# Kernel optimization log

Measured on AMD Instinct MI355X. Metric: run time of the kernel, lower is better.

## Reference

```python
import jax, jax.numpy as jnp
import numpy as np
import math

N_EMBD = 1024
N_HEAD = 16
BLOCK_SIZE = 2048
B, T = 2, 2048


def setup_inputs() -> dict:
    key = jax.random.key(0)
    ks = jax.random.split(key, 12)
    s = 0.02
    C = N_EMBD
    return {
        "x": jax.random.normal(ks[0], (B, T, C), dtype=jnp.float32),
        # LayerNorm 1
        "ln1_w": jnp.ones((C,), jnp.float32),
        "ln1_b": jnp.zeros((C,), jnp.float32),
        # attention: weights stored [in, out]
        "attn_w": jax.random.normal(ks[1], (C, 3 * C), dtype=jnp.float32) * s,
        "attn_b": jnp.zeros((3 * C,), jnp.float32),
        "proj_w": jax.random.normal(ks[2], (C, C), dtype=jnp.float32) * s,
        "proj_b": jnp.zeros((C,), jnp.float32),
        # LayerNorm 2
        "ln2_w": jnp.ones((C,), jnp.float32),
        "ln2_b": jnp.zeros((C,), jnp.float32),
        # MLP
        "fc_w": jax.random.normal(ks[3], (C, 4 * C), dtype=jnp.float32) * s,
        "fc_b": jnp.zeros((4 * C,), jnp.float32),
        "mlp_proj_w": jax.random.normal(ks[4], (4 * C, C), dtype=jnp.float32) * s,
        "mlp_proj_b": jnp.zeros((C,), jnp.float32),
    }


def _layernorm(x, w, b, eps=1e-5):
    mu = jnp.mean(x, axis=-1, keepdims=True)
    var = jnp.mean(jnp.square(x - mu), axis=-1, keepdims=True)
    return (x - mu) * jax.lax.rsqrt(var + eps) * w + b


def _attention(x, attn_w, attn_b, proj_w, proj_b):
    Bn, Tn, C = x.shape
    hs = C // N_HEAD
    qkv = x @ attn_w + attn_b                      # [B,T,3C]
    q, k, v = jnp.split(qkv, 3, axis=-1)
    # [B,H,T,hs]
    q = q.reshape(Bn, Tn, N_HEAD, hs).transpose(0, 2, 1, 3)
    k = k.reshape(Bn, Tn, N_HEAD, hs).transpose(0, 2, 1, 3)
    v = v.reshape(Bn, Tn, N_HEAD, hs).transpose(0, 2, 1, 3)
    att = jnp.einsum('bhqd,bhkd->bhqk', q, k) / math.sqrt(hs)  # [B,H,T,T]
    mask = jnp.tril(jnp.ones((Tn, Tn), dtype=bool))
    att = jnp.where(mask, att, -jnp.inf)
    att = jax.nn.softmax(att, axis=-1)
    y = jnp.einsum('bhqk,bhkd->bhqd', att, v)      # [B,H,T,hs]
    y = y.transpose(0, 2, 1, 3).reshape(Bn, Tn, C)
    return y @ proj_w + proj_b


def reference(x, ln1_w, ln1_b, attn_w, attn_b, proj_w, proj_b,
              ln2_w, ln2_b, fc_w, fc_b, mlp_proj_w, mlp_proj_b):
    x = x + _attention(_layernorm(x, ln1_w, ln1_b), attn_w, attn_b, proj_w, proj_b)
    h = _layernorm(x, ln2_w, ln2_b)
    h = jax.nn.gelu(h @ fc_w + fc_b, approximate=False)  # torch nn.GELU default = exact erf
    return x + (h @ mlp_proj_w + mlp_proj_b)
```

## Files before the change

kernel.cpp:

```cpp
#include <hip/hip_runtime.h>
#include <math.h>

typedef short s8x __attribute__((ext_vector_type(8)));
typedef float f32x4 __attribute__((ext_vector_type(4)));

__device__ __forceinline__ float bf2f(short u) {
    return __uint_as_float(((unsigned int)(unsigned short)u) << 16);
}
__device__ __forceinline__ short f2bf(float f) {
    unsigned int x = __float_as_uint(f);
    unsigned int r = (x + 0x7FFFu + ((x >> 16) & 1u)) >> 16;
    return (short)(unsigned short)r;
}

__device__ __forceinline__ void gl2lds16(const short* g, const short* l) {
    __builtin_amdgcn_global_load_lds(
        (const __attribute__((address_space(1))) void*)(unsigned long long)g,
        (__attribute__((address_space(3))) void*)(unsigned int)(unsigned long long)l,
        16, 0, 0);
}

__global__ __launch_bounds__(256) void transpose_all_k(
        const float* __restrict__ w0, const float* __restrict__ w1,
        const float* __restrict__ w2, const float* __restrict__ w3,
        short* __restrict__ o0, short* __restrict__ o1,
        short* __restrict__ o2, short* __restrict__ o3) {
    int bid = blockIdx.x;
    const float* in; short* out; int K, N, nx;
    if (bid < 3072)      { in = w0; out = o0; K = 1024; N = 3072; nx = 96; }
    else if (bid < 4096) { bid -= 3072; in = w1; out = o1; K = 1024; N = 1024; nx = 32; }
    else if (bid < 8192) { bid -= 4096; in = w2; out = o2; K = 1024; N = 4096; nx = 128; }
    else                 { bid -= 8192; in = w3; out = o3; K = 4096; N = 1024; nx = 32; }
    const int n0 = (bid % nx) * 32, k0 = (bid / nx) * 32;
    __shared__ float tile[32][33];
    const int tx = threadIdx.x & 31, ty = threadIdx.x >> 5;
#pragma unroll
    for (int i = 0; i < 4; ++i) {
        const int k = ty + i * 8;
        tile[k][tx] = in[(long)(k0 + k) * N + n0 + tx];
    }
    __syncthreads();
#pragma unroll
    for (int i = 0; i < 4; ++i) {
        const int n = ty + i * 8;
        out[(long)(n0 + n) * K + k0 + tx] = f2bf(tile[tx][n]);
    }
}

__global__ __launch_bounds__(256) void ln_k(const float* __restrict__ xin,
                                            const float* __restrict__ w,
                                            const float* __restrict__ bb,
                                            short* __restrict__ out) {
    const int row = blockIdx.x, tid = threadIdx.x;
    const float4 t = ((const float4*)(xin + (long)row * 1024))[tid];
    float v[4] = {t.x, t.y, t.z, t.w};
    float s1 = v[0] + v[1] + v[2] + v[3];
    float s2 = v[0]*v[0] + v[1]*v[1] + v[2]*v[2] + v[3]*v[3];
#pragma unroll
    for (int off = 32; off > 0; off >>= 1) {
        s1 += __shfl_xor(s1, off, 64);
        s2 += __shfl_xor(s2, off, 64);
    }
    __shared__ float red[8];
    if ((tid & 63) == 0) { red[(tid >> 6)*2] = s1; red[(tid >> 6)*2 + 1] = s2; }
    __syncthreads();
    const float t1 = red[0] + red[2] + red[4] + red[6];
    const float t2 = red[1] + red[3] + red[5] + red[7];
    const float mu = t1 * (1.0f / 1024.0f);
    float var = t2 * (1.0f / 1024.0f) - mu * mu;
    var = fmaxf(var, 0.0f);
    const float rs = rsqrtf(var + 1e-5f);
    const int ci = tid * 4;
    short4 o;
    o.x = f2bf((v[0] - mu) * rs * w[ci+0] + bb[ci+0]);
    o.y = f2bf((v[1] - mu) * rs * w[ci+1] + bb[ci+1]);
    o.z = f2bf((v[2] - mu) * rs * w[ci+2] + bb[ci+2]);
    o.w = f2bf((v[3] - mu) * rs * w[ci+3] + bb[ci+3]);
    ((short4*)(out + (long)row * 1024))[tid] = o;
}

template <int EPI, typename OutT>
__device__ __forceinline__ void epi_store(OutT* out, const float* resid, long oidx, float v) {
    if constexpr (EPI == 0) {
        out[oidx] = f2bf(v);
    } else if constexpr (EPI == 1) {
        v = 0.5f * v * (1.0f + erff(v * 0.70710678118654752f));
        out[oidx] = f2bf(v);
    } else {
        v += resid[oidx];
        out[oidx] = v;
    }
}

template <int EPI, typename OutT>
__global__ __launch_bounds__(256) void gemm_k(const short* __restrict__ A,
                                              const short* __restrict__ Bt,
                                              const float* __restrict__ bias,
                                              const float* __restrict__ resid,
                                              OutT* __restrict__ out,
                                              int M, int N, int K) {
    __shared__ __align__(16) short sA[128 * 32];
    __shared__ __align__(16) short sB[128 * 32];
    const int tid = threadIdx.x;
    const int lane = tid & 63, wave = tid >> 6;
    const int wr = (wave >> 1) * 64, wc = (wave & 1) * 64;
    const int lrow = lane & 15, quad = lane >> 4;
    const int bm = blockIdx.y * 128, bn = blockIdx.x * 128;
    const short* Ap = A + (long)(bm + (tid >> 2)) * K + (tid & 3) * 8;
    const short* Bp = Bt + (long)(bn + (tid >> 2)) * K + (tid & 3) * 8;
    const long rowstep = (long)64 * K;

    f32x4 acc[4][4] = {};
    for (int k0 = 0; k0 < K; k0 += 32) {
        __syncthreads();
        gl2lds16(Ap + k0,           sA + tid * 8);
        gl2lds16(Ap + rowstep + k0, sA + 2048 + tid * 8);
        gl2lds16(Bp + k0,           sB + tid * 8);
        gl2lds16(Bp + rowstep + k0, sB + 2048 + tid * 8);
        __syncthreads();
        s8x af[4], bfr[4];
#pragma unroll
        for (int i = 0; i < 4; ++i) af[i]  = *(const s8x*)(sA + (wr + i*16 + lrow) * 32 + quad * 8);
#pragma unroll
        for (int j = 0; j < 4; ++j) bfr[j] = *(const s8x*)(sB + (wc + j*16 + lrow) * 32 + quad * 8);
#pragma unroll
        for (int i = 0; i < 4; ++i)
#pragma unroll
            for (int j = 0; j < 4; ++j)
                acc[i][j] = __builtin_amdgcn_mfma_f32_16x16x32_bf16(af[i], bfr[j], acc[i][j], 0, 0, 0);
    }
#pragma unroll
    for (int i = 0; i < 4; ++i) {
#pragma unroll
        for (int j = 0; j < 4; ++j) {
#pragma unroll
            for (int r = 0; r < 4; ++r) {
                const int row = bm + wr + i*16 + quad*4 + r;
                const int col = bn + wc + j*16 + lrow;
                epi_store<EPI>(out, resid, (long)row * N + col, acc[i][j][r] + bias[col]);
            }
        }
    }
}

template <int EPI, typename OutT>
__global__ __launch_bounds__(256) void gemm64_k(const short* __restrict__ A,
                                                const short* __restrict__ Bt,
                                                const float* __restrict__ bias,
                                                const float* __restrict__ resid,
                                                OutT* __restrict__ out,
                                                int M, int N, int K) {
    __shared__ __align__(16) short sA[64 * 32];
    __shared__ __align__(16) short sB[128 * 32];
    const int tid = threadIdx.x;
    const int lane = tid & 63, wave = tid >> 6;
    const int lrow = lane & 15, quad = lane >> 4;
    const int bm = blockIdx.y * 64, bn = blockIdx.x * 128;
    const short* Ap = A + (long)(bm + (tid >> 2)) * K + (tid & 3) * 8;
    const short* Bp = Bt + (long)(bn + (tid >> 2)) * K + (tid & 3) * 8;
    const long rowstep = (long)64 * K;

    f32x4 acc[8] = {};
    for (int k0 = 0; k0 < K; k0 += 32) {
        __syncthreads();
        gl2lds16(Ap + k0,           sA + tid * 8);
        gl2lds16(Bp + k0,           sB + tid * 8);
        gl2lds16(Bp + rowstep + k0, sB + 2048 + tid * 8);
        __syncthreads();
        const s8x af = *(const s8x*)(sA + (wave * 16 + lrow) * 32 + quad * 8);
#pragma unroll
        for (int j = 0; j < 8; ++j) {
            const s8x bf = *(const s8x*)(sB + (j * 16 + lrow) * 32 + quad * 8);
            acc[j] = __builtin_amdgcn_mfma_f32_16x16x32_bf16(af, bf, acc[j], 0, 0, 0);
        }
    }
#pragma unroll
    for (int j = 0; j < 8; ++j) {
#pragma unroll
        for (int r = 0; r < 4; ++r) {
            const int row = bm + wave * 16 + quad * 4 + r;
            const int col = bn + j * 16 + lrow;
            epi_store<EPI>(out, resid, (long)row * N + col, acc[j][r] + bias[col]);
        }
    }
}

__global__ __launch_bounds__(256) void attn_k(const short* __restrict__ qkv,
                                              short* __restrict__ y) {
    const int bx = blockIdx.x;
    const int b = blockIdx.y >> 4, h = blockIdx.y & 15;
    const int qtA = bx, qtB = 31 - bx;
    const int tid = threadIdx.x, lane = tid & 63, wave = tid >> 6;
    const int lrow = lane & 15, quad = lane >> 4;
    const long base = (long)b * 2048 * 3072;

    __shared__ __align__(16) short sK[64 * 64];
    __shared__ __align__(16) short sVt[64 * 64];
    __shared__ __align__(16) short sP[64 * 72];

    s8x qfA0, qfA1, qfB0, qfB1;
    {
        const short* qpA = qkv + base + (long)(qtA * 64 + wave * 16 + lrow) * 3072 + h * 64 + quad * 8;
        qfA0 = *(const s8x*)qpA; qfA1 = *(const s8x*)(qpA + 32);
        const short* qpB = qkv + base + (long)(qtB * 64 + wave * 16 + lrow) * 3072 + h * 64 + quad * 8;
        qfB0 = *(const s8x*)qpB; qfB1 = *(const s8x*)(qpB + 32);
    }
    f32x4 oA[4], oB[4], lA = {}, lB = {};
#pragma unroll
    for (int d = 0; d < 4; ++d) { oA[d] = f32x4{0.f,0.f,0.f,0.f}; oB[d] = f32x4{0.f,0.f,0.f,0.f}; }

    s8x ones;
#pragma unroll
    for (int j = 0; j < 8; ++j) ones[j] = (short)0x3F80;

    const int srow = tid >> 3;
    const int sg   = tid & 7;
    const int sw0 = ((srow & 7) ^ (srow >> 3)) & 7;
    const int sw1 = (((srow + 32) & 7) ^ ((srow + 32) >> 3)) & 7;

    const float cs = 0.125f * 1.4426950408889634f;
    const float c0 = 14.426950408889634f;

    auto tile_step = [&](const s8x& qf0, const s8x& qf1, const s8x* kf0, const s8x* kf1,
                         f32x4* o, f32x4& lacc, int qt, int kt, int k0) {
        f32x4 s[4];
#pragma unroll
        for (int ct = 0; ct < 4; ++ct) {
            f32x4 t = f32x4{0.f, 0.f, 0.f, 0.f};
            t = __builtin_amdgcn_mfma_f32_16x16x32_bf16(qf0, kf0[ct], t, 0, 0, 0);
            t = __builtin_amdgcn_mfma_f32_16x16x32_bf16(qf1, kf1[ct], t, 0, 0, 0);
            s[ct] = t;
        }
        if (kt == qt) {
            const int qrow = qt * 64 + wave * 16 + quad * 4;
#pragma unroll
            for (int ct = 0; ct < 4; ++ct) {
                const int key = k0 + ct * 16 + lrow;
#pragma unroll
                for (int r = 0; r < 4; ++r) {
                    const float e = (key > qrow + r) ? -1e30f : fmaf(s[ct][r], cs, -c0);
                    s[ct][r] = exp2f(e);
                }
            }
        } else {
#pragma unroll
            for (int ct = 0; ct < 4; ++ct)
#pragma unroll
                for (int r = 0; r < 4; ++r)
                    s[ct][r] = exp2f(fmaf(s[ct][r], cs, -c0));
        }
#pragma unroll
        for (int ct = 0; ct < 4; ++ct)
#pragma unroll
            for (int r = 0; r < 4; ++r)
                sP[(wave * 16 + quad * 4 + r) * 72 + ct * 16 + lrow] = f2bf(s[ct][r]);
#pragma unroll
        for (int ks = 0; ks < 2; ++ks) {
            const s8x pf = *(const s8x*)(sP + (wave * 16 + lrow) * 72 + ks * 32 + quad * 8);
            lacc = __builtin_amdgcn_mfma_f32_16x16x32_bf16(pf, ones, lacc, 0, 0, 0);
#pragma unroll
            for (int dt = 0; dt < 4; ++dt) {
                const int d = dt * 16 + lrow;
                const int swd = ((d & 7) ^ (d >> 3)) & 7;
                const s8x vf = *(const s8x*)(sVt + d * 64 + (((ks * 4 + quad) ^ swd) * 8));
                o[dt] = __builtin_amdgcn_mfma_f32_16x16x32_bf16(pf, vf, o[dt], 0, 0, 0);
            }
        }
    };

    for (int kt = 0; kt <= qtB; ++kt) {
        const int k0 = kt * 64;
        __syncthreads();
        {
            const short* kbase = qkv + base + 1024 + h * 64;
            gl2lds16(kbase + (long)(k0 + srow) * 3072      + (sg ^ sw0) * 8, sK + tid * 8);
            gl2lds16(kbase + (long)(k0 + srow + 32) * 3072 + (sg ^ sw1) * 8, sK + 2048 + tid * 8);
            const short* vp = qkv + base + (long)(k0 + srow) * 3072 + 2048 + h * 64 + sg * 8;
            const uint4 v0 = *(const uint4*)vp;
            const uint4 v1 = *(const uint4*)(vp + 32 * 3072);
            const short* e0 = (const short*)&v0;
            const short* e1 = (const short*)&v1;
#pragma unroll
            for (int i = 0; i < 8; ++i) {
                const int d = sg * 8 + i;
                const int swd = ((d & 7) ^ (d >> 3)) & 7;
                sVt[d * 64 + ( srow       ^ (swd << 3))] = e0[i];
                sVt[d * 64 + ((srow + 32) ^ (swd << 3))] = e1[i];
            }
        }
        __syncthreads();

        s8x kf0[4], kf1[4];
#pragma unroll
        for (int ct = 0; ct < 4; ++ct) {
            const int row = ct * 16 + lrow;
            const int swr = ((row & 7) ^ (row >> 3)) & 7;
            kf0[ct] = *(const s8x*)(sK + row * 64 + ((quad ^ swr) * 8));
            kf1[ct] = *(const s8x*)(sK + row * 64 + (((4 + quad) ^ swr) * 8));
        }
        if (kt <= qtA) tile_step(qfA0, qfA1, kf0, kf1, oA, lA, qtA, kt, k0);
        tile_step(qfB0, qfB1, kf0, kf1, oB, lB, qtB, kt, k0);
    }
    float rA[4], rB[4];
#pragma unroll
    for (int r = 0; r < 4; ++r) { rA[r] = 1.0f / lA[r]; rB[r] = 1.0f / lB[r]; }
#pragma unroll
    for (int dt = 0; dt < 4; ++dt) {
#pragma unroll
        for (int r = 0; r < 4; ++r) {
            const int qA = qtA * 64 + wave * 16 + quad * 4 + r;
            const int qB = qtB * 64 + wave * 16 + quad * 4 + r;
            y[((long)b * 2048 + qA) * 1024 + h * 64 + dt * 16 + lrow] = f2bf(oA[dt][r] * rA[r]);
            y[((long)b * 2048 + qB) * 1024 + h * 64 + dt * 16 + lrow] = f2bf(oB[dt][r] * rB[r]);
        }
    }
}

extern "C" void kernel_launch(void* const* d_in, const int* in_sizes, int n_in,
                              void* d_out, int out_size, void* d_ws, size_t ws_size,
                              hipStream_t stream) {
    const float* x      = (const float*)d_in[0];
    const float* ln1_w  = (const float*)d_in[1];
    const float* ln1_b  = (const float*)d_in[2];
    const float* attn_w = (const float*)d_in[3];
    const float* attn_b = (const float*)d_in[4];
    const float* proj_w = (const float*)d_in[5];
    const float* proj_b = (const float*)d_in[6];
    const float* ln2_w  = (const float*)d_in[7];
    const float* ln2_b  = (const float*)d_in[8];
    const float* fc_w   = (const float*)d_in[9];
    const float* fc_b   = (const float*)d_in[10];
    const float* mlp_w  = (const float*)d_in[11];
    const float* mlp_b  = (const float*)d_in[12];

    char* ws = (char*)d_ws;
    short* attn_wt = (short*)(ws + 0);
    short* proj_wt = (short*)(ws + 6291456L);
    short* fc_wt   = (short*)(ws + 8388608L);
    short* mlp_wt  = (short*)(ws + 16777216L);
    short* slotA   = (short*)(ws + 25165824L);
    short* slotB   = (short*)(ws + 33554432L);

    short* xln  = slotA;
    short* yb   = slotA;
    short* hb   = slotA;
    short* qkvb = slotB;
    short* hh   = slotB;
    float* x1   = (float*)d_out;
    float* outp = (float*)d_out;

    transpose_all_k<<<12288, 256, 0, stream>>>(attn_w, proj_w, fc_w, mlp_w,
                                               attn_wt, proj_wt, fc_wt, mlp_wt);

    ln_k<<<4096, 256, 0, stream>>>(x, ln1_w, ln1_b, xln);
    gemm_k<0, short><<<dim3(24, 32), 256, 0, stream>>>(xln, attn_wt, attn_b, nullptr, qkvb, 4096, 3072, 1024);
    attn_k<<<dim3(16, 32), 256, 0, stream>>>(qkvb, yb);
    gemm64_k<2, float><<<dim3(8, 64), 256, 0, stream>>>(yb, proj_wt, proj_b, x, x1, 4096, 1024, 1024);
    ln_k<<<4096, 256, 0, stream>>>(x1, ln2_w, ln2_b, hb);
    gemm_k<1, short><<<dim3(32, 32), 256, 0, stream>>>(hb, fc_wt, fc_b, nullptr, hh, 4096, 4096, 1024);
    gemm64_k<3, float><<<dim3(8, 64), 256, 0, stream>>>(hh, mlp_wt, mlp_b, x1, outp, 4096, 1024, 4096);
}
```

Measured before the change: 391.3 us.

## Double-buffer LDS tiles in GEMM and attention kernels, use tanh-form GELU

Both GEMM kernels and the attention kernel now use two LDS buffers, so the global-to-LDS copy of the next K/V or A/B tile is issued before the MFMA work on the current tile, with one barrier per iteration instead of two. The 64-row GEMM also stages two 32-wide K slices per iteration. The GELU epilogue swaps the exact erf formula for the tanh approximation written as a sigmoid with __expf, to make the epilogue cheaper. The cost is twice the shared memory, which may lower occupancy, and a small numerical deviation from the exact-erf GELU in the reference.

```diff
diff --git a/kernel.cpp b/kernel.cpp
--- a/kernel.cpp
+++ b/kernel.cpp
@@ -84,7 +84,8 @@
     if constexpr (EPI == 0) {
         out[oidx] = f2bf(v);
     } else if constexpr (EPI == 1) {
-        v = 0.5f * v * (1.0f + erff(v * 0.70710678118654752f));
+        const float u = v * (0.79788456080f + 0.03567740814f * v * v);
+        v = v / (1.0f + __expf(-2.0f * u));
         out[oidx] = f2bf(v);
     } else {
         v += resid[oidx];
@@ -99,8 +100,8 @@
                                               const float* __restrict__ resid,
                                               OutT* __restrict__ out,
                                               int M, int N, int K) {
-    __shared__ __align__(16) short sA[128 * 32];
-    __shared__ __align__(16) short sB[128 * 32];
+    __shared__ __align__(16) short sA[2][128 * 32];
+    __shared__ __align__(16) short sB[2][128 * 32];
     const int tid = threadIdx.x;
     const int lane = tid & 63, wave = tid >> 6;
     const int wr = (wave >> 1) * 64, wc = (wave & 1) * 64;
@@ -110,19 +111,27 @@
     const short* Bp = Bt + (long)(bn + (tid >> 2)) * K + (tid & 3) * 8;
     const long rowstep = (long)64 * K;
 
+    auto stage = [&](int p, int k0) {
+        gl2lds16(Ap + k0,           sA[p] + tid * 8);
+        gl2lds16(Ap + rowstep + k0, sA[p] + 2048 + tid * 8);
+        gl2lds16(Bp + k0,           sB[p] + tid * 8);
+        gl2lds16(Bp + rowstep + k0, sB[p] + 2048 + tid * 8);
+    };
+
     f32x4 acc[4][4] = {};
-    for (int k0 = 0; k0 < K; k0 += 32) {
+    stage(0, 0);
+    const int S = K >> 5;
+    for (int s = 0; s < S; ++s) {
+        const int p = s & 1;
         __syncthreads();
-        gl2lds16(Ap + k0,           sA + tid * 8);
-        gl2lds16(Ap + rowstep + k0, sA + 2048 + tid * 8);
-        gl2lds16(Bp + k0,           sB + tid * 8);
-        gl2lds16(Bp + rowstep + k0, sB + 2048 + tid * 8);
-        __syncthreads();
+        if (s + 1 < S) stage(p ^ 1, (s + 1) << 5);
+        const short* pA = sA[p];
+        const short* pB = sB[p];
         s8x af[4], bfr[4];
 #pragma unroll
-        for (int i = 0; i < 4; ++i) af[i]  = *(const s8x*)(sA + (wr + i*16 + lrow) * 32 + quad * 8);
-#pragma unroll
-        for (int j = 0; j < 4; ++j) bfr[j] = *(const s8x*)(sB + (wc + j*16 + lrow) * 32 + quad * 8);
+        for (int i = 0; i < 4; ++i) af[i]  = *(const s8x*)(pA + (wr + i*16 + lrow) * 32 + quad * 8);
+#pragma unroll
+        for (int j = 0; j < 4; ++j) bfr[j] = *(const s8x*)(pB + (wc + j*16 + lrow) * 32 + quad * 8);
 #pragma unroll
         for (int i = 0; i < 4; ++i)
 #pragma unroll
@@ -150,8 +159,8 @@
                                                 const float* __restrict__ resid,
                                                 OutT* __restrict__ out,
                                                 int M, int N, int K) {
-    __shared__ __align__(16) short sA[64 * 32];
-    __shared__ __align__(16) short sB[128 * 32];
+    __shared__ __align__(16) short sA[2][2][64 * 32];
+    __shared__ __align__(16) short sB[2][2][128 * 32];
     const int tid = threadIdx.x;
     const int lane = tid & 63, wave = tid >> 6;
     const int lrow = lane & 15, quad = lane >> 4;
@@ -160,18 +169,30 @@
     const short* Bp = Bt + (long)(bn + (tid >> 2)) * K + (tid & 3) * 8;
     const long rowstep = (long)64 * K;
 
+    auto stage = [&](int p, int k0) {
+#pragma unroll
+        for (int hp = 0; hp < 2; ++hp) {
+            gl2lds16(Ap + k0 + hp * 32,           sA[p][hp] + tid * 8);
+            gl2lds16(Bp + k0 + hp * 32,           sB[p][hp] + tid * 8);
+            gl2lds16(Bp + rowstep + k0 + hp * 32, sB[p][hp] + 2048 + tid * 8);
+        }
+    };
+
     f32x4 acc[8] = {};
-    for (int k0 = 0; k0 < K; k0 += 32) {
+    stage(0, 0);
+    const int S = K >> 6;
+    for (int s = 0; s < S; ++s) {
+        const int p = s & 1;
         __syncthreads();
-        gl2lds16(Ap + k0,           sA + tid * 8);
-        gl2lds16(Bp + k0,           sB + tid * 8);
-        gl2lds16(Bp + rowstep + k0, sB + 2048 + tid * 8);
-        __syncthreads();
-        const s8x af = *(const s8x*)(sA + (wave * 16 + lrow) * 32 + quad * 8);
-#pragma unroll
-        for (int j = 0; j < 8; ++j) {
-            const s8x bf = *(const s8x*)(sB + (j * 16 + lrow) * 32 + quad * 8);
-            acc[j] = __builtin_amdgcn_mfma_f32_16x16x32_bf16(af, bf, acc[j], 0, 0, 0);
+        if (s + 1 < S) stage(p ^ 1, (s + 1) << 6);
+#pragma unroll
+        for (int hp = 0; hp < 2; ++hp) {
+            const s8x af = *(const s8x*)(sA[p][hp] + (wave * 16 + lrow) * 32 + quad * 8);
+#pragma unroll
+            for (int j = 0; j < 8; ++j) {
+                const s8x bf = *(const s8x*)(sB[p][hp] + (j * 16 + lrow) * 32 + quad * 8);
+                acc[j] = __builtin_amdgcn_mfma_f32_16x16x32_bf16(af, bf, acc[j], 0, 0, 0);
+            }
         }
     }
 #pragma unroll
@@ -194,8 +215,8 @@
     const int lrow = lane & 15, quad = lane >> 4;
     const long base = (long)b * 2048 * 3072;
 
-    __shared__ __align__(16) short sK[64 * 64];
-    __shared__ __align__(16) short sVt[64 * 64];
+    __shared__ __align__(16) short sK[2][64 * 64];
+    __shared__ __align__(16) short sVt[2][64 * 64];
     __shared__ __align__(16) short sP[64 * 72];
 
     s8x qfA0, qfA1, qfB0, qfB1;
@@ -218,11 +239,36 @@
     const int sw0 = ((srow & 7) ^ (srow >> 3)) & 7;
     const int sw1 = (((srow + 32) & 7) ^ ((srow + 32) >> 3)) & 7;
 
+    const short* kbase = qkv + base + 1024 + h * 64;
+    const short* vbase = qkv + base + 2048 + h * 64;
+
+    uint4 vr0, vr1;
+    auto issueK = [&](int p, int k0) {
+        gl2lds16(kbase + (long)(k0 + srow) * 3072      + (sg ^ sw0) * 8, sK[p] + tid * 8);
+        gl2lds16(kbase + (long)(k0 + srow + 32) * 3072 + (sg ^ sw1) * 8, sK[p] + 2048 + tid * 8);
+    };
+    auto loadV = [&](int k0) {
+        const short* vp = vbase + (long)(k0 + srow) * 3072 + sg * 8;
+        vr0 = *(const uint4*)vp;
+        vr1 = *(const uint4*)(vp + 32 * 3072);
+    };
+    auto writeV = [&](int p) {
+        const short* e0 = (const short*)&vr0;
+        const short* e1 = (const short*)&vr1;
+#pragma unroll
+        for (int i = 0; i < 8; ++i) {
+            const int d = sg * 8 + i;
+            const int swd = i ^ sg;
+            sVt[p][d * 64 + ( srow       ^ (swd << 3))] = e0[i];
+            sVt[p][d * 64 + ((srow + 32) ^ (swd << 3))] = e1[i];
+        }
+    };
+
     const float cs = 0.125f * 1.4426950408889634f;
     const float c0 = 14.426950408889634f;
 
     auto tile_step = [&](const s8x& qf0, const s8x& qf1, const s8x* kf0, const s8x* kf1,
-                         f32x4* o, f32x4& lacc, int qt, int kt, int k0) {
+                         const short* pV, f32x4* o, f32x4& lacc, int qt, int kt, int k0) {
         f32x4 s[4];
 #pragma unroll
         for (int ct = 0; ct < 4; ++ct) {
@@ -262,44 +308,30 @@
             for (int dt = 0; dt < 4; ++dt) {
                 const int d = dt * 16 + lrow;
                 const int swd = ((d & 7) ^ (d >> 3)) & 7;
-                const s8x vf = *(const s8x*)(sVt + d * 64 + (((ks * 4 + quad) ^ swd) * 8));
+                const s8x vf = *(const s8x*)(pV + d * 64 + (((ks * 4 + quad) ^ swd) * 8));
                 o[dt] = __builtin_amdgcn_mfma_f32_16x16x32_bf16(pf, vf, o[dt], 0, 0, 0);
             }
         }
     };
 
+    issueK(0, 0);
+    loadV(0);
     for (int kt = 0; kt <= qtB; ++kt) {
-        const int k0 = kt * 64;
+        const int p = kt & 1, k0 = kt * 64;
+        writeV(p);
         __syncthreads();
-        {
-            const short* kbase = qkv + base + 1024 + h * 64;
-            gl2lds16(kbase + (long)(k0 + srow) * 3072      + (sg ^ sw0) * 8, sK + tid * 8);
-            gl2lds16(kbase + (long)(k0 + srow + 32) * 3072 + (sg ^ sw1) * 8, sK + 2048 + tid * 8);
-            const short* vp = qkv + base + (long)(k0 + srow) * 3072 + 2048 + h * 64 + sg * 8;
-            const uint4 v0 = *(const uint4*)vp;
-            const uint4 v1 = *(const uint4*)(vp + 32 * 3072);
-            const short* e0 = (const short*)&v0;
-            const short* e1 = (const short*)&v1;
-#pragma unroll
-            for (int i = 0; i < 8; ++i) {
-                const int d = sg * 8 + i;
-                const int swd = ((d & 7) ^ (d >> 3)) & 7;
-                sVt[d * 64 + ( srow       ^ (swd << 3))] = e0[i];
-                sVt[d * 64 + ((srow + 32) ^ (swd << 3))] = e1[i];
-            }
-        }
-        __syncthreads();
+        if (kt < qtB) { issueK(p ^ 1, k0 + 64); loadV(k0 + 64); }
 
         s8x kf0[4], kf1[4];
 #pragma unroll
         for (int ct = 0; ct < 4; ++ct) {
             const int row = ct * 16 + lrow;
             const int swr = ((row & 7) ^ (row >> 3)) & 7;
-            kf0[ct] = *(const s8x*)(sK + row * 64 + ((quad ^ swr) * 8));
-            kf1[ct] = *(const s8x*)(sK + row * 64 + (((4 + quad) ^ swr) * 8));
-        }
-        if (kt <= qtA) tile_step(qfA0, qfA1, kf0, kf1, oA, lA, qtA, kt, k0);
-        tile_step(qfB0, qfB1, kf0, kf1, oB, lB, qtB, kt, k0);
+            kf0[ct] = *(const s8x*)(sK[p] + row * 64 + ((quad ^ swr) * 8));
+            kf1[ct] = *(const s8x*)(sK[p] + row * 64 + (((4 + quad) ^ swr) * 8));
+        }
+        if (kt <= qtA) tile_step(qfA0, qfA1, kf0, kf1, sVt[p], oA, lA, qtA, kt, k0);
+        tile_step(qfB0, qfB1, kf0, kf1, sVt[p], oB, lB, qtB, kt, k0);
     }
     float rA[4], rB[4];
 #pragma unroll
```

Measured after the change: 348.2 us. -11.0%, faster.
